# Optimization experiments

Hardware: AMD Instinct MI355X
Metric: run time of the kernel (lower is better)

The kernel has to match this reference:

```python
import jax, jax.numpy as jnp
import numpy as np

R = 32768          # rays
S = 128            # fixed step budget per ray (padded/masked)
STEP = 0.02        # step_size
NX = NY = NZ = 256
MINB = jnp.array([-1.0, -1.0, -1.0], jnp.float32)
MAXB = jnp.array([1.0, 1.0, 1.0], jnp.float32)
# voxel sizes: (max - min) / (n - 1)
VOX = (MAXB - MINB) / (jnp.array([NX, NY, NZ], jnp.float32) - 1.0)
N = jnp.array([NX, NY, NZ], jnp.int32)
# 8 corner offsets, same order as the original query_voxels
OFFS = jnp.array([[0,0,0],[1,0,0],[0,1,0],[1,1,0],
                  [0,0,1],[1,0,1],[0,1,1],[1,1,1]], jnp.int32)


def setup_inputs() -> dict:
    key = jax.random.key(0)
    k1, k2, k3 = jax.random.split(key, 3)
    origins = jax.random.uniform(k1, (R, 3), jnp.float32, -0.9, 0.9)
    d = jax.random.normal(k2, (R, 3), jnp.float32)
    directions = d / jnp.linalg.norm(d, axis=-1, keepdims=True)
    sdf_values = jax.random.normal(k3, (NX, NY, NZ), jnp.float32)
    return {"origins": origins, "directions": directions, "sdf_values": sdf_values}


def reference(origins, directions, sdf_values):
    # --- ray_box_intersection (faithful, including the tmin reuse in tmax) ---
    inv_dir = 1.0 / directions                       # [R,3]
    a = (MINB - origins) * inv_dir                   # [R,3]
    b = (MAXB - origins) * inv_dir                   # [R,3]
    t0 = jnp.max(jnp.minimum(a, b), axis=-1)         # [R] scalar tmin
    t1 = jnp.min(jnp.maximum(t0[:, None], b), axis=-1)  # [R] (original overwrites tmin first)
    hit = t1 >= t0                                   # original returns None if tmax < tmin

    # --- march_ray: fixed step grid t = t_near + i*step, masked at t >= t_far ---
    t = t0[:, None] + STEP * jnp.arange(S, dtype=jnp.float32)   # [R,S]
    step_mask = (t < t1[:, None]) & hit[:, None]                # [R,S]
    pts = origins[:, None, :] + t[..., None] * directions[:, None, :]  # [R,S,3]

    # --- query_voxels: truncating index like torch .long() ---
    idx = ((pts - MINB) / VOX).astype(jnp.int32)                # [R,S,3]
    inb = jnp.all((idx >= 0) & (idx < N - 1), axis=-1)          # [R,S]
    valid = inb & step_mask                                     # [R,S]
    idxc = jnp.clip(idx, 0, N - 2)                              # safe gather indices
    ci = idxc[:, :, None, :] + OFFS                             # [R,S,8,3]
    sdf = sdf_values[ci[..., 0], ci[..., 1], ci[..., 2]]        # [R,S,8] 8-corner gather
    sdf = jnp.where(valid[..., None], sdf, 0.0)
    positions = MINB + ci.astype(jnp.float32) * VOX             # [R,S,8,3] corner positions
    positions = jnp.where(valid[..., None, None], positions, 0.0)
    return sdf, positions, valid
```

## Files before the change

### kernel.cpp

```cpp
#include <hip/hip_runtime.h>


constexpr int   RAYS = 32768;
constexpr int   STEPS = 128;
constexpr float STEP = 0.02f;
constexpr float VOX = 2.0f / 255.0f;

typedef float f4 __attribute__((ext_vector_type(4)));
typedef float f2 __attribute__((ext_vector_type(2), aligned(4)));

__global__ __launch_bounds__(256, 8) void sdf_march_kernel(
    const float* __restrict__ org,
    const float* __restrict__ dir,
    const float* __restrict__ sdfv,
    float* __restrict__ out_sdf,
    float* __restrict__ out_pos,
    float* __restrict__ out_valid)
{
#pragma clang fp contract(off)
    __shared__ f4 lds_pos[768];
    __shared__ f4 lds_sdf[512];

    const int tid = threadIdx.x;
    const int gid = blockIdx.x * 256 + tid;
    const int r = gid >> 7;
    const int s = gid & 127;

    const float ox = org[r * 3 + 0], oy = org[r * 3 + 1], oz = org[r * 3 + 2];
    const float dx = dir[r * 3 + 0], dy = dir[r * 3 + 1], dz = dir[r * 3 + 2];

    const float ivx = 1.0f / dx, ivy = 1.0f / dy, ivz = 1.0f / dz;
    const float axv = (-1.0f - ox) * ivx, ayv = (-1.0f - oy) * ivy, azv = (-1.0f - oz) * ivz;
    const float bxv = ( 1.0f - ox) * ivx, byv = ( 1.0f - oy) * ivy, bzv = ( 1.0f - oz) * ivz;
    const float t0 = fmaxf(fmaxf(fminf(axv, bxv), fminf(ayv, byv)), fminf(azv, bzv));
    const float t1 = fminf(fminf(fmaxf(t0, bxv), fmaxf(t0, byv)), fmaxf(t0, bzv));
    const bool hit = (t1 >= t0);

    const float ts = STEP * (float)s;
    const float t  = t0 + ts;
    const bool step_mask = (t < t1) && hit;

    const float mx = t * dx, my = t * dy, mz = t * dz;
    const float px = ox + mx, py = oy + my, pz = oz + mz;

    const float fx = (px + 1.0f) / VOX;
    const float fy = (py + 1.0f) / VOX;
    const float fz = (pz + 1.0f) / VOX;
    const int ix = (int)fx, iy = (int)fy, iz = (int)fz;
    const bool inb = (ix >= 0) & (ix < 255) & (iy >= 0) & (iy < 255) & (iz >= 0) & (iz < 255);
    const bool valid = inb && step_mask;

    const int ixc = min(max(ix, 0), 254);
    const int iyc = min(max(iy, 0), 254);
    const int izc = min(max(iz, 0), 254);

    f4 sv0 = {0.f, 0.f, 0.f, 0.f}, sv1 = {0.f, 0.f, 0.f, 0.f};
    float x0 = 0.f, x1 = 0.f, y0 = 0.f, y1 = 0.f, z0 = 0.f, z1 = 0.f;

    if (valid) {
        const int base = (ixc * 256 + iyc) * 256 + izc;
        const f2 vz00 = *(const f2*)(sdfv + base);
        const f2 vz10 = *(const f2*)(sdfv + base + 65536);
        const f2 vz01 = *(const f2*)(sdfv + base + 256);
        const f2 vz11 = *(const f2*)(sdfv + base + 65536 + 256);
        sv0 = (f4){vz00.x, vz10.x, vz01.x, vz11.x};
        sv1 = (f4){vz00.y, vz10.y, vz01.y, vz11.y};

        x0 = -1.0f + (float)ixc * VOX;
        x1 = -1.0f + (float)(ixc + 1) * VOX;
        y0 = -1.0f + (float)iyc * VOX;
        y1 = -1.0f + (float)(iyc + 1) * VOX;
        z0 = -1.0f + (float)izc * VOX;
        z1 = -1.0f + (float)(izc + 1) * VOX;
    }

    const int lrec = tid & 127;
    const bool lowHalf = (tid < 128);

    lds_sdf[tid * 2 + 0] = sv0;
    lds_sdf[tid * 2 + 1] = sv1;
    if (lowHalf) {
        f4* lp = lds_pos + lrec * 6;
        lp[0] = (f4){x0, y0, z0, x1};
        lp[1] = (f4){y0, z0, x0, y1};
        lp[2] = (f4){z0, x1, y1, z0};
        lp[3] = (f4){x0, y0, z1, x1};
        lp[4] = (f4){y0, z1, x0, y1};
        lp[5] = (f4){z1, x1, y1, z1};
    }

    __builtin_nontemporal_store(valid ? 1.0f : 0.0f, out_valid + gid);

    __syncthreads();

    f4* os = (f4*)out_sdf + (size_t)blockIdx.x * 512;
    __builtin_nontemporal_store(lds_sdf[tid],       os + tid);
    __builtin_nontemporal_store(lds_sdf[tid + 256], os + tid + 256);

    f4* op = (f4*)out_pos + (size_t)blockIdx.x * 1536;
#pragma unroll
    for (int k = 0; k < 3; ++k) {
        __builtin_nontemporal_store(lds_pos[tid + 256 * k], op + tid + 256 * k);
    }

    __syncthreads();

    if (!lowHalf) {
        f4* lp = lds_pos + lrec * 6;
        lp[0] = (f4){x0, y0, z0, x1};
        lp[1] = (f4){y0, z0, x0, y1};
        lp[2] = (f4){z0, x1, y1, z0};
        lp[3] = (f4){x0, y0, z1, x1};
        lp[4] = (f4){y0, z1, x0, y1};
        lp[5] = (f4){z1, x1, y1, z1};
    }

    __syncthreads();

#pragma unroll
    for (int k = 0; k < 3; ++k) {
        __builtin_nontemporal_store(lds_pos[tid + 256 * k], op + 768 + tid + 256 * k);
    }
}

extern "C" void kernel_launch(void* const* d_in, const int* in_sizes, int n_in,
                              void* d_out, int out_size, void* d_ws, size_t ws_size,
                              hipStream_t stream) {
    const float* origins    = (const float*)d_in[0];
    const float* directions = (const float*)d_in[1];
    const float* sdf_values = (const float*)d_in[2];

    float* out = (float*)d_out;
    float* out_sdf   = out;
    float* out_pos   = out + 33554432;
    float* out_valid = out + 33554432 + 100663296;

    const int total = RAYS * STEPS;
    dim3 grid(total / 256), block(256);
    sdf_march_kernel<<<grid, block, 0, stream>>>(origins, directions, sdf_values,
                                                 out_sdf, out_pos, out_valid);
}
```

Baseline: 602.5 us.

## Stage full position tile in LDS once and overlap gather latency with position stores

Doubles the LDS position buffer so all 256 threads write their corner positions in one pass, removing the two-phase half-block staging and one barrier. Position stores are issued before the SDF gather results are consumed, so the gather latency can overlap with streaming the position output. LDS use rises to about 32 KB per block and the occupancy hint in launch bounds is dropped, which may reduce resident blocks per CU.

```diff
diff --git a/kernel.cpp b/kernel.cpp
--- a/kernel.cpp
+++ b/kernel.cpp
@@ -9,7 +9,7 @@
 typedef float f4 __attribute__((ext_vector_type(4)));
 typedef float f2 __attribute__((ext_vector_type(2), aligned(4)));
 
-__global__ __launch_bounds__(256, 8) void sdf_march_kernel(
+__global__ __launch_bounds__(256) void sdf_march_kernel(
     const float* __restrict__ org,
     const float* __restrict__ dir,
     const float* __restrict__ sdfv,
@@ -18,7 +18,7 @@
     float* __restrict__ out_valid)
 {
 #pragma clang fp contract(off)
-    __shared__ f4 lds_pos[768];
+    __shared__ f4 lds_pos[1536];
     __shared__ f4 lds_sdf[512];
 
     const int tid = threadIdx.x;
@@ -54,18 +54,17 @@
     const int iyc = min(max(iy, 0), 254);
     const int izc = min(max(iz, 0), 254);
 
-    f4 sv0 = {0.f, 0.f, 0.f, 0.f}, sv1 = {0.f, 0.f, 0.f, 0.f};
-    float x0 = 0.f, x1 = 0.f, y0 = 0.f, y1 = 0.f, z0 = 0.f, z1 = 0.f;
-
+    f2 vz00 = {0.f, 0.f}, vz10 = {0.f, 0.f}, vz01 = {0.f, 0.f}, vz11 = {0.f, 0.f};
     if (valid) {
         const int base = (ixc * 256 + iyc) * 256 + izc;
-        const f2 vz00 = *(const f2*)(sdfv + base);
-        const f2 vz10 = *(const f2*)(sdfv + base + 65536);
-        const f2 vz01 = *(const f2*)(sdfv + base + 256);
-        const f2 vz11 = *(const f2*)(sdfv + base + 65536 + 256);
-        sv0 = (f4){vz00.x, vz10.x, vz01.x, vz11.x};
-        sv1 = (f4){vz00.y, vz10.y, vz01.y, vz11.y};
+        vz00 = *(const f2*)(sdfv + base);
+        vz10 = *(const f2*)(sdfv + base + 65536);
+        vz01 = *(const f2*)(sdfv + base + 256);
+        vz11 = *(const f2*)(sdfv + base + 65536 + 256);
+    }
 
+    float x0 = 0.f, x1 = 0.f, y0 = 0.f, y1 = 0.f, z0 = 0.f, z1 = 0.f;
+    if (valid) {
         x0 = -1.0f + (float)ixc * VOX;
         x1 = -1.0f + (float)(ixc + 1) * VOX;
         y0 = -1.0f + (float)iyc * VOX;
@@ -74,53 +73,34 @@
         z1 = -1.0f + (float)(izc + 1) * VOX;
     }
 
-    const int lrec = tid & 127;
-    const bool lowHalf = (tid < 128);
+    f4* lp = lds_pos + tid * 6;
+    lp[0] = (f4){x0, y0, z0, x1};
+    lp[1] = (f4){y0, z0, x0, y1};
+    lp[2] = (f4){z0, x1, y1, z0};
+    lp[3] = (f4){x0, y0, z1, x1};
+    lp[4] = (f4){y0, z1, x0, y1};
+    lp[5] = (f4){z1, x1, y1, z1};
 
+    __builtin_nontemporal_store(valid ? 1.0f : 0.0f, out_valid + gid);
+
+    __syncthreads();
+
+    f4* op = (f4*)out_pos + (size_t)blockIdx.x * 1536;
+#pragma unroll
+    for (int k = 0; k < 6; ++k) {
+        __builtin_nontemporal_store(lds_pos[tid + 256 * k], op + tid + 256 * k);
+    }
+
+    const f4 sv0 = (f4){vz00.x, vz10.x, vz01.x, vz11.x};
+    const f4 sv1 = (f4){vz00.y, vz10.y, vz01.y, vz11.y};
     lds_sdf[tid * 2 + 0] = sv0;
     lds_sdf[tid * 2 + 1] = sv1;
-    if (lowHalf) {
-        f4* lp = lds_pos + lrec * 6;
-        lp[0] = (f4){x0, y0, z0, x1};
-        lp[1] = (f4){y0, z0, x0, y1};
-        lp[2] = (f4){z0, x1, y1, z0};
-        lp[3] = (f4){x0, y0, z1, x1};
-        lp[4] = (f4){y0, z1, x0, y1};
-        lp[5] = (f4){z1, x1, y1, z1};
-    }
-
-    __builtin_nontemporal_store(valid ? 1.0f : 0.0f, out_valid + gid);
 
     __syncthreads();
 
     f4* os = (f4*)out_sdf + (size_t)blockIdx.x * 512;
     __builtin_nontemporal_store(lds_sdf[tid],       os + tid);
     __builtin_nontemporal_store(lds_sdf[tid + 256], os + tid + 256);
-
-    f4* op = (f4*)out_pos + (size_t)blockIdx.x * 1536;
-#pragma unroll
-    for (int k = 0; k < 3; ++k) {
-        __builtin_nontemporal_store(lds_pos[tid + 256 * k], op + tid + 256 * k);
-    }
-
-    __syncthreads();
-
-    if (!lowHalf) {
-        f4* lp = lds_pos + lrec * 6;
-        lp[0] = (f4){x0, y0, z0, x1};
-        lp[1] = (f4){y0, z0, x0, y1};
-        lp[2] = (f4){z0, x1, y1, z0};
-        lp[3] = (f4){x0, y0, z1, x1};
-        lp[4] = (f4){y0, z1, x0, y1};
-        lp[5] = (f4){z1, x1, y1, z1};
-    }
-
-    __syncthreads();
-
-#pragma unroll
-    for (int k = 0; k < 3; ++k) {
-        __builtin_nontemporal_store(lds_pos[tid + 256 * k], op + 768 + tid + 256 * k);
-    }
 }
 
 extern "C" void kernel_launch(void* const* d_in, const int* in_sizes, int n_in,
```

Measured after the change: 592.8 us, median of 2. About the same (-1.6%).
